# Kernel optimization log

Hardware: AMD Instinct MI355X
Metric: run time of the kernel (lower is better)

Reference implementation:

```python
import jax, jax.numpy as jnp
import numpy as np

D = 1024      # d_model
H = 16        # num_heads
HW = D // H   # head_width = 64
FF = 4 * D    # hidden_dim = 4096
BATCH = 2
T = 2048
EPS = 1e-5


def layer_norm(x, g, b):
    mu = jnp.mean(x, axis=-1, keepdims=True)
    var = jnp.mean(jnp.square(x - mu), axis=-1, keepdims=True)
    return (x - mu) * jax.lax.rsqrt(var + EPS) * g + b


def setup_inputs() -> dict:
    key = jax.random.key(0)
    ks = jax.random.split(key, 7)
    s = 0.02
    return {
        "x": jax.random.normal(ks[0], (BATCH, T, D), dtype=jnp.float32),
        "Wq": jax.random.normal(ks[1], (D, D), dtype=jnp.float32) * s,
        "Wk": jax.random.normal(ks[2], (D, D), dtype=jnp.float32) * s,
        "Wv": jax.random.normal(ks[3], (D, D), dtype=jnp.float32) * s,
        "W1": jax.random.normal(ks[4], (FF, D), dtype=jnp.float32) * s,
        "W2": jax.random.normal(ks[5], (D, FF), dtype=jnp.float32) * s,
        "g1": jnp.ones((D,), dtype=jnp.float32),
        "b1": jnp.zeros((D,), dtype=jnp.float32),
        "g2": jnp.ones((D,), dtype=jnp.float32),
        "b2": jnp.zeros((D,), dtype=jnp.float32),
    }


def reference(x, Wq, Wk, Wv, W1, W2, g1, b1, g2, b2):
    N, t, d = x.shape
    # norm1
    xn = layer_norm(x, g1, b1)

    # --- MHSA with ALiBi + causal mask (math mirrors torch module) ---
    def heads(y):  # (N,t,D) -> (N,H,t,HW)
        return y.reshape(N, t, H, HW).transpose(0, 2, 1, 3)

    q = heads(xn @ Wq.T)
    k = heads(xn @ Wk.T)
    v = heads(xn @ Wv.T)

    scores = jnp.einsum("nhqd,nhkd->nhqk", q, k) / np.sqrt(HW).astype(np.float32)

    pos = jnp.arange(t)
    rel = (pos[None, :] - pos[:, None]).astype(x.dtype)           # [t,t], rel[i,j]=j-i
    slopes = (2.0 ** (-(jnp.arange(1, H + 1)) * (8.0 / H))).astype(x.dtype)  # [H]
    alibi = slopes[:, None, None] * rel                            # [H,t,t]
    causal = jnp.where(pos[None, :] > pos[:, None],
                       jnp.array(-jnp.inf, x.dtype),
                       jnp.array(0.0, x.dtype))                    # [t,t]

    att = jax.nn.softmax(scores + alibi[None] + causal[None, None], axis=-1)
    o = jnp.einsum("nhqk,nhkd->nhqd", att, v)
    o = o.transpose(0, 2, 1, 3).reshape(N, t, d)

    att_out = xn + o

    # --- MLP: Linear -> SiLU -> Linear ---
    h = layer_norm(att_out, g2, b2)
    m = jax.nn.silu(h @ W1.T) @ W2.T
    return att_out + m
```

## Files before the change

kernel.cpp:

```cpp
#include <hip/hip_runtime.h>

#define DMODEL 1024
#define NHEAD  16
#define HWID   64
#define FFDIM  4096
#define NBATCH 2
#define SEQT   2048
#define NTOK   4096
#define QKLD   3072

using bf8    = __attribute__((ext_vector_type(8))) short;
using f32x4  = __attribute__((ext_vector_type(4))) float;
using f32x16 = __attribute__((ext_vector_type(16))) float;

__device__ inline short to_bf16(float f) {
  unsigned u = __float_as_uint(f);
  return (short)((u + 0x7fffu + ((u >> 16) & 1u)) >> 16);
}
__device__ inline float from_bf16(short s) {
  return __uint_as_float(((unsigned)(unsigned short)s) << 16);
}
__device__ inline float exp2_fast(float x) {
  float r;
  asm("v_exp_f32 %0, %1" : "=v"(r) : "v"(x));
  return r;
}
__device__ inline unsigned cvt_pk_bf16(float lo, float hi) {
  unsigned r;
  asm("v_cvt_pk_bf16_f32 %0, %1, %2" : "=v"(r) : "v"(lo), "v"(hi));
  return r;
}
__device__ inline void lds_load16(const void* g, void* l) {
  __builtin_amdgcn_global_load_lds(
      (const __attribute__((address_space(1))) void*)g,
      (__attribute__((address_space(3))) void*)l, 16, 0, 0);
}

__global__ __launch_bounds__(256)
void cvt_all(const float* __restrict__ Wq, const float* __restrict__ Wk,
             const float* __restrict__ Wv, const float* __restrict__ W1,
             const float* __restrict__ W2, short* __restrict__ wqkv,
             short* __restrict__ w1b, short* __restrict__ w2b) {
  int i = blockIdx.x * 256 + threadIdx.x;
  const float* src;
  short* dst;
  if (i < 1048576)      { src = W1; dst = w1b; }
  else if (i < 2097152) { src = W2; dst = w2b;            i -= 1048576; }
  else if (i < 2359296) { src = Wq; dst = wqkv;           i -= 2097152; }
  else if (i < 2621440) { src = Wk; dst = wqkv + 1048576; i -= 2359296; }
  else                  { src = Wv; dst = wqkv + 2097152; i -= 2621440; }
  float4 v = ((const float4*)src)[i];
  short4 o;
  o.x = to_bf16(v.x); o.y = to_bf16(v.y);
  o.z = to_bf16(v.z); o.w = to_bf16(v.w);
  ((short4*)dst)[i] = o;
}

__global__ __launch_bounds__(256)
void ln_kernel(const float* __restrict__ x, const float* __restrict__ g,
               const float* __restrict__ b, short* __restrict__ out) {
  const int row = blockIdx.x;
  const int t = threadIdx.x;
  const float4 v = ((const float4*)(x + (long)row * DMODEL))[t];
  float s  = v.x + v.y + v.z + v.w;
  float s2 = v.x * v.x + v.y * v.y + v.z * v.z + v.w * v.w;
#pragma unroll
  for (int m = 1; m < 64; m <<= 1) {
    s  += __shfl_xor(s, m);
    s2 += __shfl_xor(s2, m);
  }
  __shared__ float red[8];
  if ((t & 63) == 0) { red[t >> 6] = s; red[4 + (t >> 6)] = s2; }
  __syncthreads();
  s  = red[0] + red[1] + red[2] + red[3];
  s2 = red[4] + red[5] + red[6] + red[7];
  const float mu = s * (1.f / DMODEL);
  const float rs = rsqrtf(s2 * (1.f / DMODEL) - mu * mu + 1e-5f);
  const float4 gv = ((const float4*)g)[t];
  const float4 bv = ((const float4*)b)[t];
  short4 o;
  o.x = to_bf16((v.x - mu) * rs * gv.x + bv.x);
  o.y = to_bf16((v.y - mu) * rs * gv.y + bv.y);
  o.z = to_bf16((v.z - mu) * rs * gv.z + bv.z);
  o.w = to_bf16((v.w - mu) * rs * gv.w + bv.w);
  ((short4*)(out + (long)row * DMODEL))[t] = o;
}

template <int EPI>
__global__ __launch_bounds__(256, 2)
void gemm4(const short* __restrict__ A, const short* __restrict__ Bw,
           void* __restrict__ Cout, int N, int lda, int ldb, int Kslice,
           long zstride) {
  __shared__ short lds[3][12288];
  const int tid = threadIdx.x;
  const int w = tid >> 6, lane = tid & 63;
  const int l15 = lane & 15, l4 = lane >> 4;
  const int wm = w >> 1, wn = w & 1;

  const int gx = gridDim.x, nwg = gx * gridDim.y;
  const int wg = blockIdx.y * gx + blockIdx.x;
  const int sw = (wg & 7) * (nwg >> 3) + (wg >> 3);
  const int sx = gx >> 2;
  const int st = sw >> 4, w16 = sw & 15;
  const long bm = (long)((st / sx) * 4 + (w16 >> 2)) * 256;
  const long bn = (long)((st % sx) * 4 + (w16 & 3)) * 128;
  const long kofs = (long)blockIdx.z * Kslice;

  long aoff[4], boff[2];
#pragma unroll
  for (int i = 0; i < 4; ++i) {
    const int c = i * 4 + w;
    const int row = c * 16 + (lane >> 2);
    const int slog = (lane & 3) ^ ((row >> 1) & 3);
    aoff[i] = (bm + row) * (long)lda + slog * 8 + kofs;
  }
#pragma unroll
  for (int i = 0; i < 2; ++i) {
    const int c = i * 4 + w;
    const int row = c * 16 + (lane >> 2);
    const int slog = (lane & 3) ^ ((row >> 1) & 3);
    boff[i] = (bn + row) * (long)ldb + slog * 8 + kofs;
  }
  int offA[8], offB[4];
#pragma unroll
  for (int m = 0; m < 8; ++m) {
    const int row = wm * 128 + m * 16 + l15;
    offA[m] = row * 64 + ((l4 ^ ((row >> 1) & 3)) << 4);
  }
#pragma unroll
  for (int n = 0; n < 4; ++n) {
    const int row = wn * 64 + n * 16 + l15;
    offB[n] = row * 64 + ((l4 ^ ((row >> 1) & 3)) << 4);
  }

  const int NT = Kslice >> 5;
  f32x4 acc[8][4] = {};

#pragma unroll
  for (int t = 0; t < 2; ++t) {
    char* db = (char*)&lds[t][0];
#pragma unroll
    for (int i = 0; i < 4; ++i)
      lds_load16(A + aoff[i] + t * 32, db + (i * 4 + w) * 1024);
#pragma unroll
    for (int i = 0; i < 2; ++i)
      lds_load16(Bw + boff[i] + t * 32, db + 16384 + (i * 4 + w) * 1024);
  }

  int slot = 0, pslot = 2;
  for (int t = 0; t < NT; ++t) {
    if (t + 1 < NT) asm volatile("s_waitcnt vmcnt(6)" ::: "memory");
    else            asm volatile("s_waitcnt vmcnt(0)" ::: "memory");
    __builtin_amdgcn_s_barrier();
    asm volatile("" ::: "memory");
    if (t + 2 < NT) {
      char* db = (char*)&lds[pslot][0];
      const long ks = (long)(t + 2) * 32;
#pragma unroll
      for (int i = 0; i < 4; ++i)
        lds_load16(A + aoff[i] + ks, db + (i * 4 + w) * 1024);
#pragma unroll
      for (int i = 0; i < 2; ++i)
        lds_load16(Bw + boff[i] + ks, db + 16384 + (i * 4 + w) * 1024);
    }
    const char* sb = (const char*)&lds[slot][0];
    bf8 af[8], bfr[4];
#pragma unroll
    for (int m = 0; m < 8; ++m) af[m] = *(const bf8*)(sb + offA[m]);
#pragma unroll
    for (int n = 0; n < 4; ++n) bfr[n] = *(const bf8*)(sb + 16384 + offB[n]);
    __builtin_amdgcn_s_setprio(1);
#pragma unroll
    for (int m = 0; m < 8; ++m)
#pragma unroll
      for (int n = 0; n < 4; ++n)
        acc[m][n] = __builtin_amdgcn_mfma_f32_16x16x32_bf16(af[m], bfr[n], acc[m][n], 0, 0, 0);
    __builtin_amdgcn_s_setprio(0);
    slot  = (slot  == 2) ? 0 : slot  + 1;
    pslot = (pslot == 2) ? 0 : pslot + 1;
  }

  float* Cp = (float*)Cout + (EPI == 2 ? (long)blockIdx.z * zstride : 0);
#pragma unroll
  for (int m = 0; m < 8; ++m)
#pragma unroll
    for (int n = 0; n < 4; ++n) {
      const long col = bn + wn * 64 + n * 16 + l15;
#pragma unroll
      for (int r = 0; r < 4; ++r) {
        const long row = bm + wm * 128 + m * 16 + l4 * 4 + r;
        float v = acc[m][n][r];
        if (EPI == 0) {
          ((short*)Cout)[row * N + col] = to_bf16(v);
        } else if (EPI == 1) {
          ((short*)Cout)[row * N + col] = to_bf16(v / (1.f + __expf(-v)));
        } else {
          Cp[row * N + col] = v;
        }
      }
    }
}

__global__ __launch_bounds__(256)
void pack_kv(const short* __restrict__ qkv, short* __restrict__ Kp,
             short* __restrict__ Vp) {
  __shared__ short tile[64][72];
  const int bx = blockIdx.x, bh = blockIdx.y;
  const int b = bh >> 4, h = bh & 15;
  const int t = threadIdx.x;
  if (bx < 64) {
    const int g = bx;
    const int row = t >> 3, cc = t & 7, c = cc >> 1, hi = cc & 1;
    const bf8 v = *(const bf8*)&qkv[(long)(b * SEQT + g * 32 + row) * QKLD +
                                    1024 + h * HWID + c * 16 + hi * 8];
    *(bf8*)&Kp[(((long)bh * 256 + g * 4 + c) * 64 + hi * 32 + row) * 8] = v;
  } else {
    const int tc = bx - 64;
    {
      const int r = t >> 2, c = (t & 3) * 16;
      const long src = (long)(b * SEQT + tc * 64 + r) * QKLD + 2048 + h * HWID + c;
      *(bf8*)&tile[r][c]     = *(const bf8*)&qkv[src];
      *(bf8*)&tile[r][c + 8] = *(const bf8*)&qkv[src + 8];
    }
    __syncthreads();
    const int dg = t >> 7, ch = (t >> 5) & 3, row = t & 31;
#pragma unroll
    for (int hi = 0; hi < 2; ++hi) {
      short o[8];
#pragma unroll
      for (int j = 0; j < 8; ++j) o[j] = tile[ch * 16 + hi * 8 + j][dg * 32 + row];
      *(bf8*)&Vp[(((long)bh * 256 + dg * 128 + tc * 4 + ch) * 64 + hi * 32 + row) * 8] =
          *(bf8*)o;
    }
  }
}

__global__ __launch_bounds__(64, 2)
void attn_kernel(const short* __restrict__ qkv, const short* __restrict__ Kp,
                 const short* __restrict__ Vp, const short* __restrict__ xn,
                 float* __restrict__ att) {
  const int L = blockIdx.x;
  const int bh = (L & 7) * 4 + ((L >> 3) & 3);
  const int qtile = 63 - (L >> 5);
  const int b = bh >> 4, h = bh & 15;
  const int q0 = qtile * 32;
  const int lane = threadIdx.x;
  const int l31 = lane & 31, hi = lane >> 5;
  const long tokbase = (long)b * SEQT;

  bf8 qf[4];
  {
    const short* qrow = qkv + (tokbase + q0 + l31) * QKLD + h * HWID + hi * 8;
#pragma unroll
    for (int c = 0; c < 4; ++c) qf[c] = *(const bf8*)(qrow + c * 16);
  }

  const float slope2 = exp2f(-0.5f * (float)(h + 1)) * 1.44269504f;
  const float sc2 = 0.125f * 1.44269504f;
  float arr[16];
#pragma unroll
  for (int r = 0; r < 16; ++r) arr[r] = slope2 * (float)((r & 3) + 8 * (r >> 2));
  const float hofs = slope2 * 4.f * (float)hi;
  const float qabs = (float)(q0 + l31);

  float m2 = -1e30f, lsum = 0.f;
  f32x16 acc0 = {}, acc1 = {};
  const int ktm = q0 >> 6;
  const bf8* kfb = (const bf8*)Kp + (long)bh * 16384 + lane;
  const bf8* vfb = (const bf8*)Vp + (long)bh * 16384 + lane;

  bf8 kc[8], kn[8], vc[8];
#pragma unroll
  for (int c = 0; c < 4; ++c) {
    kc[c]     = kfb[c * 64];
    kc[4 + c] = kfb[256 + c * 64];
  }

#pragma unroll 2
  for (int kt = 0; kt <= ktm; ++kt) {
    const int k0 = kt * 64;
    const long vb = (long)kt * 256;
#pragma unroll
    for (int ch = 0; ch < 4; ++ch) {
      vc[ch]     = vfb[vb + ch * 64];
      vc[4 + ch] = vfb[8192 + vb + ch * 64];
    }
    const long nb = (long)(kt < ktm ? kt + 1 : kt) * 512;
#pragma unroll
    for (int c = 0; c < 4; ++c) {
      kn[c]     = kfb[nb + c * 64];
      kn[4 + c] = kfb[nb + 256 + c * 64];
    }
    f32x16 s0 = {}, s1 = {};
#pragma unroll
    for (int c = 0; c < 4; ++c) {
      s0 = __builtin_amdgcn_mfma_f32_32x32x16_bf16(kc[c], qf[c], s0, 0, 0, 0);
      s1 = __builtin_amdgcn_mfma_f32_32x32x16_bf16(kc[4 + c], qf[c], s1, 0, 0, 0);
    }
    const float base = slope2 * ((float)k0 - qabs) + hofs;
    float s[32];
#pragma unroll
    for (int r = 0; r < 16; ++r) {
      s[r]      = fmaf(s0[r], sc2, base + arr[r]);
      s[16 + r] = fmaf(s1[r], sc2, base + arr[r] + slope2 * 32.f);
    }
    if (kt == ktm) {
      const int qi = q0 + l31;
#pragma unroll
      for (int r = 0; r < 16; ++r) {
        const int krel = (r & 3) + 8 * (r >> 2) + 4 * hi;
        if (k0 + krel > qi)      s[r]      = -1e30f;
        if (k0 + 32 + krel > qi) s[16 + r] = -1e30f;
      }
    }
    float ma = s[0], mb = s[1], mc = s[2], md = s[3];
#pragma unroll
    for (int i = 4; i < 32; i += 4) {
      ma = fmaxf(ma, s[i]); mb = fmaxf(mb, s[i + 1]);
      mc = fmaxf(mc, s[i + 2]); md = fmaxf(md, s[i + 3]);
    }
    float pm = fmaxf(fmaxf(ma, mb), fmaxf(mc, md));
    pm = fmaxf(pm, __shfl_xor(pm, 32));
    if (!__all(pm - m2 <= 11.0f)) {
      const float nm = fmaxf(m2, pm);
      const float alpha = exp2_fast(m2 - nm);
      m2 = nm;
      lsum *= alpha;
      acc0 *= alpha;
      acc1 *= alpha;
    }
    float p[32];
#pragma unroll
    for (int i = 0; i < 32; ++i) p[i] = exp2_fast(s[i] - m2);
    float sa = p[0], sb = p[1], sc = p[2], sd = p[3];
#pragma unroll
    for (int i = 4; i < 32; i += 4) {
      sa += p[i]; sb += p[i + 1]; sc += p[i + 2]; sd += p[i + 3];
    }
    float rs = (sa + sb) + (sc + sd);
    rs += __shfl_xor(rs, 32);
    lsum += rs;
    unsigned cpk[16];
#pragma unroll
    for (int g = 0; g < 8; ++g) {
      cpk[g]     = cvt_pk_bf16(p[2 * g], p[2 * g + 1]);
      cpk[8 + g] = cvt_pk_bf16(p[16 + 2 * g], p[16 + 2 * g + 1]);
    }
    bf8 pb[4];
#pragma unroll
    for (int ch = 0; ch < 4; ++ch) {
      const int cb = (ch >> 1) * 8 + (ch & 1) * 4;
      unsigned u0 = cpk[cb + 0], u2 = cpk[cb + 2];
      unsigned u1 = cpk[cb + 1], u3 = cpk[cb + 3];
      asm("v_permlane32_swap_b32 %0, %1" : "+v"(u0), "+v"(u2));
      asm("v_permlane32_swap_b32 %0, %1" : "+v"(u1), "+v"(u3));
      union { unsigned u[4]; bf8 v; } f;
      f.u[0] = u0; f.u[1] = u1; f.u[2] = u2; f.u[3] = u3;
      pb[ch] = f.v;
    }
#pragma unroll
    for (int ch = 0; ch < 4; ++ch) {
      acc0 = __builtin_amdgcn_mfma_f32_32x32x16_bf16(vc[ch], pb[ch], acc0, 0, 0, 0);
      acc1 = __builtin_amdgcn_mfma_f32_32x32x16_bf16(vc[4 + ch], pb[ch], acc1, 0, 0, 0);
    }
#pragma unroll
    for (int i = 0; i < 8; ++i) kc[i] = kn[i];
  }

  __shared__ float Os[32 * 68];
  const float rl = 1.f / lsum;
#pragma unroll
  for (int r = 0; r < 16; ++r) {
    const int d0 = (r & 3) + 8 * (r >> 2) + 4 * hi;
    Os[l31 * 68 + d0]      = acc0[r] * rl;
    Os[l31 * 68 + 32 + d0] = acc1[r] * rl;
  }
  __syncthreads();
#pragma unroll
  for (int it = 0; it < 8; ++it) {
    const int idx = it * 64 + lane;
    const int row = idx >> 4, c4 = idx & 15;
    const float4 ov = *(const float4*)&Os[row * 68 + c4 * 4];
    const long gbase = (tokbase + q0 + row) * DMODEL + h * HWID + c4 * 4;
    const short4 xv = *(const short4*)&xn[gbase];
    float4 o;
    o.x = ov.x + from_bf16(xv.x);
    o.y = ov.y + from_bf16(xv.y);
    o.z = ov.z + from_bf16(xv.z);
    o.w = ov.w + from_bf16(xv.w);
    *(float4*)&att[gbase] = o;
  }
}

__global__ __launch_bounds__(256)
void combine_kernel(const float* __restrict__ p, float* __restrict__ dout, int n4) {
  int i = blockIdx.x * 256 + threadIdx.x;
  if (i < n4) {
    float4 a  = ((const float4*)dout)[i];
    float4 b0 = ((const float4*)(p))[i];
    float4 b1 = ((const float4*)(p + 4194304))[i];
    float4 b2 = ((const float4*)(p + 8388608))[i];
    float4 b3 = ((const float4*)(p + 12582912))[i];
    a.x += (b0.x + b1.x) + (b2.x + b3.x);
    a.y += (b0.y + b1.y) + (b2.y + b3.y);
    a.z += (b0.z + b1.z) + (b2.z + b3.z);
    a.w += (b0.w + b1.w) + (b2.w + b3.w);
    ((float4*)dout)[i] = a;
  }
}

extern "C" void kernel_launch(void* const* d_in, const int* in_sizes, int n_in,
                              void* d_out, int out_size, void* d_ws, size_t ws_size,
                              hipStream_t stream) {
  (void)in_sizes; (void)n_in; (void)out_size; (void)ws_size;
  const float* x  = (const float*)d_in[0];
  const float* Wq = (const float*)d_in[1];
  const float* Wk = (const float*)d_in[2];
  const float* Wv = (const float*)d_in[3];
  const float* W1 = (const float*)d_in[4];
  const float* W2 = (const float*)d_in[5];
  const float* g1 = (const float*)d_in[6];
  const float* b1 = (const float*)d_in[7];
  const float* g2 = (const float*)d_in[8];
  const float* b2 = (const float*)d_in[9];

  char* ws = (char*)d_ws;
  const size_t MB = 1024 * 1024;
  short* wqkv_b = (short*)(ws + 0);
  short* w1_b   = (short*)(ws + 6  * MB);
  short* w2_b   = (short*)(ws + 14 * MB);
  short* xn     = (short*)(ws + 22 * MB);
  short* qkv    = (short*)(ws + 30 * MB);
  short* m1     = (short*)(ws + 22 * MB);
  short* Kp     = (short*)(ws + 54 * MB);
  short* Vp     = (short*)(ws + 62 * MB);
  short* hb     = (short*)(ws + 70 * MB);
  float* parts  = (float*)(ws + 54 * MB);
  float* att    = (float*)d_out;

  cvt_all<<<11264, 256, 0, stream>>>(Wq, Wk, Wv, W1, W2, wqkv_b, w1_b, w2_b);

  ln_kernel<<<NTOK, 256, 0, stream>>>(x, g1, b1, xn);

  gemm4<0><<<dim3(24, 16), 256, 0, stream>>>(xn, wqkv_b, qkv, QKLD, DMODEL, DMODEL,
                                             DMODEL, 0);
  pack_kv<<<dim3(96, 32), 256, 0, stream>>>(qkv, Kp, Vp);

  attn_kernel<<<2048, 64, 0, stream>>>(qkv, Kp, Vp, xn, att);

  ln_kernel<<<NTOK, 256, 0, stream>>>(att, g2, b2, hb);

  gemm4<1><<<dim3(32, 16), 256, 0, stream>>>(hb, w1_b, m1, FFDIM, DMODEL, DMODEL,
                                             DMODEL, 0);
  gemm4<2><<<dim3(8, 16, 4), 256, 0, stream>>>(m1, w2_b, parts, DMODEL, FFDIM, FFDIM,
                                               1024, (long)NTOK * DMODEL);
  combine_kernel<<<4096, 256, 0, stream>>>(parts, (float*)d_out, 1048576);
}
```

Measured before the change: 205.0 us.

## Switch GEMMs to 512-thread 256x256 tiles with 4-stage LDS ring and register double-buffering

The GEMM kernel now uses 8 waves per workgroup, each computing a 256x256 output tile instead of 256x128, which halves the number of workgroups per GEMM. The LDS ring grows from 3 to 4 stages so global prefetches run three K-steps ahead. LDS fragments for step t+1 are loaded into alternate register sets while the MFMAs for step t execute. The aim is more operand reuse per tile and better overlap of loads with compute. In exchange, register pressure and LDS use go up (128KB per workgroup), and the smaller grids may leave CUs idle.

```diff
diff --git a/kernel.cpp b/kernel.cpp
--- a/kernel.cpp
+++ b/kernel.cpp
@@ -87,15 +87,15 @@
 }
 
 template <int EPI>
-__global__ __launch_bounds__(256, 2)
-void gemm4(const short* __restrict__ A, const short* __restrict__ Bw,
-           void* __restrict__ Cout, int N, int lda, int ldb, int Kslice,
-           long zstride) {
-  __shared__ short lds[3][12288];
+__global__ __launch_bounds__(512, 2)
+void gemm8r(const short* __restrict__ A, const short* __restrict__ Bw,
+            void* __restrict__ Cout, int N, int lda, int ldb, int Kslice,
+            long zstride) {
+  __shared__ short lds[4][16384];
   const int tid = threadIdx.x;
-  const int w = tid >> 6, lane = tid & 63;
+  const int wid = tid >> 6, lane = tid & 63;
   const int l15 = lane & 15, l4 = lane >> 4;
-  const int wm = w >> 1, wn = w & 1;
+  const int wm = wid >> 2, wn = wid & 3;
 
   const int gx = gridDim.x, nwg = gx * gridDim.y;
   const int wg = blockIdx.y * gx + blockIdx.x;
@@ -103,23 +103,19 @@
   const int sx = gx >> 2;
   const int st = sw >> 4, w16 = sw & 15;
   const long bm = (long)((st / sx) * 4 + (w16 >> 2)) * 256;
-  const long bn = (long)((st % sx) * 4 + (w16 & 3)) * 128;
+  const long bn = (long)((st % sx) * 4 + (w16 & 3)) * 256;
   const long kofs = (long)blockIdx.z * Kslice;
 
-  long aoff[4], boff[2];
-#pragma unroll
-  for (int i = 0; i < 4; ++i) {
-    const int c = i * 4 + w;
-    const int row = c * 16 + (lane >> 2);
-    const int slog = (lane & 3) ^ ((row >> 1) & 3);
-    aoff[i] = (bm + row) * (long)lda + slog * 8 + kofs;
-  }
-#pragma unroll
-  for (int i = 0; i < 2; ++i) {
-    const int c = i * 4 + w;
-    const int row = c * 16 + (lane >> 2);
-    const int slog = (lane & 3) ^ ((row >> 1) & 3);
-    boff[i] = (bn + row) * (long)ldb + slog * 8 + kofs;
+  long aoff[2], boff[2];
+  int  doff[2];
+#pragma unroll
+  for (int l = 0; l < 2; ++l) {
+    const int gid = l * 512 + tid;
+    const int row = gid >> 2;
+    const int sg = (gid & 3) ^ ((row >> 1) & 3);
+    aoff[l] = (bm + row) * (long)lda + kofs + sg * 8;
+    boff[l] = (bn + row) * (long)ldb + kofs + sg * 8;
+    doff[l] = gid * 16;
   }
   int offA[8], offB[4];
 #pragma unroll
@@ -135,49 +131,63 @@
 
   const int NT = Kslice >> 5;
   f32x4 acc[8][4] = {};
-
-#pragma unroll
-  for (int t = 0; t < 2; ++t) {
-    char* db = (char*)&lds[t][0];
-#pragma unroll
-    for (int i = 0; i < 4; ++i)
-      lds_load16(A + aoff[i] + t * 32, db + (i * 4 + w) * 1024);
-#pragma unroll
-    for (int i = 0; i < 2; ++i)
-      lds_load16(Bw + boff[i] + t * 32, db + 16384 + (i * 4 + w) * 1024);
-  }
-
-  int slot = 0, pslot = 2;
-  for (int t = 0; t < NT; ++t) {
-    if (t + 1 < NT) asm volatile("s_waitcnt vmcnt(6)" ::: "memory");
+  bf8 fa0[8], fb0[4], fa1[8], fb1[4];
+
+#pragma unroll
+  for (int tt = 0; tt < 3; ++tt) {
+    char* db = (char*)&lds[tt][0];
+#pragma unroll
+    for (int l = 0; l < 2; ++l) {
+      lds_load16(A  + aoff[l] + tt * 32, db + doff[l]);
+      lds_load16(Bw + boff[l] + tt * 32, db + 16384 + doff[l]);
+    }
+  }
+  asm volatile("s_waitcnt vmcnt(8)" ::: "memory");
+  __builtin_amdgcn_s_barrier();
+  asm volatile("" ::: "memory");
+  {
+    const char* sb = (const char*)&lds[0][0];
+#pragma unroll
+    for (int m = 0; m < 8; ++m) fa0[m] = *(const bf8*)(sb + offA[m]);
+#pragma unroll
+    for (int n = 0; n < 4; ++n) fb0[n] = *(const bf8*)(sb + 16384 + offB[n]);
+  }
+
+  auto step = [&](int t, bf8 (&ca)[8], bf8 (&cb)[4],
+                  bf8 (&na)[8], bf8 (&nb)[4]) {
+    if (t + 3 < NT) asm volatile("s_waitcnt vmcnt(4)" ::: "memory");
     else            asm volatile("s_waitcnt vmcnt(0)" ::: "memory");
     __builtin_amdgcn_s_barrier();
     asm volatile("" ::: "memory");
-    if (t + 2 < NT) {
-      char* db = (char*)&lds[pslot][0];
-      const long ks = (long)(t + 2) * 32;
-#pragma unroll
-      for (int i = 0; i < 4; ++i)
-        lds_load16(A + aoff[i] + ks, db + (i * 4 + w) * 1024);
-#pragma unroll
-      for (int i = 0; i < 2; ++i)
-        lds_load16(Bw + boff[i] + ks, db + 16384 + (i * 4 + w) * 1024);
-    }
-    const char* sb = (const char*)&lds[slot][0];
-    bf8 af[8], bfr[4];
-#pragma unroll
-    for (int m = 0; m < 8; ++m) af[m] = *(const bf8*)(sb + offA[m]);
-#pragma unroll
-    for (int n = 0; n < 4; ++n) bfr[n] = *(const bf8*)(sb + 16384 + offB[n]);
+    if (t + 3 < NT) {
+      char* db = (char*)&lds[(t + 3) & 3][0];
+      const long ks = (long)(t + 3) * 32;
+#pragma unroll
+      for (int l = 0; l < 2; ++l) {
+        lds_load16(A  + aoff[l] + ks, db + doff[l]);
+        lds_load16(Bw + boff[l] + ks, db + 16384 + doff[l]);
+      }
+    }
+    if (t + 1 < NT) {
+      const char* sb = (const char*)&lds[(t + 1) & 3][0];
+#pragma unroll
+      for (int m = 0; m < 8; ++m) na[m] = *(const bf8*)(sb + offA[m]);
+#pragma unroll
+      for (int n = 0; n < 4; ++n) nb[n] = *(const bf8*)(sb + 16384 + offB[n]);
+    }
+    __builtin_amdgcn_sched_barrier(0);
     __builtin_amdgcn_s_setprio(1);
 #pragma unroll
     for (int m = 0; m < 8; ++m)
 #pragma unroll
       for (int n = 0; n < 4; ++n)
-        acc[m][n] = __builtin_amdgcn_mfma_f32_16x16x32_bf16(af[m], bfr[n], acc[m][n], 0, 0, 0);
+        acc[m][n] = __builtin_amdgcn_mfma_f32_16x16x32_bf16(ca[m], cb[n], acc[m][n], 0, 0, 0);
     __builtin_amdgcn_s_setprio(0);
-    slot  = (slot  == 2) ? 0 : slot  + 1;
-    pslot = (pslot == 2) ? 0 : pslot + 1;
+  };
+
+  for (int t = 0; t < NT; t += 2) {
+    step(t,     fa0, fb0, fa1, fb1);
+    step(t + 1, fa1, fb1, fa0, fb0);
   }
 
   float* Cp = (float*)Cout + (EPI == 2 ? (long)blockIdx.z * zstride : 0);
@@ -442,17 +452,17 @@
 
   ln_kernel<<<NTOK, 256, 0, stream>>>(x, g1, b1, xn);
 
-  gemm4<0><<<dim3(24, 16), 256, 0, stream>>>(xn, wqkv_b, qkv, QKLD, DMODEL, DMODEL,
-                                             DMODEL, 0);
+  gemm8r<0><<<dim3(12, 16), 512, 0, stream>>>(xn, wqkv_b, qkv, QKLD, DMODEL, DMODEL,
+                                              DMODEL, 0);
   pack_kv<<<dim3(96, 32), 256, 0, stream>>>(qkv, Kp, Vp);
 
   attn_kernel<<<2048, 64, 0, stream>>>(qkv, Kp, Vp, xn, att);
 
   ln_kernel<<<NTOK, 256, 0, stream>>>(att, g2, b2, hb);
 
-  gemm4<1><<<dim3(32, 16), 256, 0, stream>>>(hb, w1_b, m1, FFDIM, DMODEL, DMODEL,
-                                             DMODEL, 0);
-  gemm4<2><<<dim3(8, 16, 4), 256, 0, stream>>>(m1, w2_b, parts, DMODEL, FFDIM, FFDIM,
-                                               1024, (long)NTOK * DMODEL);
+  gemm8r<1><<<dim3(16, 16), 512, 0, stream>>>(hb, w1_b, m1, FFDIM, DMODEL, DMODEL,
+                                              DMODEL, 0);
+  gemm8r<2><<<dim3(4, 16, 4), 512, 0, stream>>>(m1, w2_b, parts, DMODEL, FFDIM, FFDIM,
+                                                1024, (long)NTOK * DMODEL);
   combine_kernel<<<4096, 256, 0, stream>>>(parts, (float*)d_out, 1048576);
 }
```

Result: no change. 204.8 us (-0.1%).
